# Optimization experiments

Measured on AMD Instinct MI355X. Metric: run time of the kernel, lower is better.

Reference implementation:

```python
import jax, jax.numpy as jnp
import numpy as np

# Production-scale dims (RecSys CTR): huge batch, modest feature dim -> memory-bound.
BATCH = 262144
DIM = 128
NUM_DOMAIN = 8
EPS = 1e-3  # Keras BatchNormalization default epsilon


def setup_inputs() -> dict:
    key = jax.random.key(0)
    k1, k2 = jax.random.split(key)
    inputs = jax.random.normal(k1, (BATCH, DIM), dtype=jnp.float32)
    domain_index = jax.random.randint(k2, (BATCH,), 0, NUM_DOMAIN, dtype=jnp.int32)
    # Learned params, matching Constant(0.5)/Zeros initializers in build().
    global_gamma = jnp.full((DIM,), 0.5, dtype=jnp.float32)
    global_beta = jnp.zeros((DIM,), dtype=jnp.float32)
    domain_gamma = jnp.full((NUM_DOMAIN, DIM), 0.5, dtype=jnp.float32)
    domain_beta = jnp.zeros((NUM_DOMAIN, DIM), dtype=jnp.float32)
    return {
        "inputs": inputs,
        "global_gamma": global_gamma,
        "global_beta": global_beta,
        "domain_gamma": domain_gamma,
        "domain_beta": domain_beta,
        "domain_index": domain_index,
    }


def reference(inputs, global_gamma, global_beta, domain_gamma, domain_beta, domain_index):
    """Partitioned Normalization (training-mode BN stats per domain).

    Equivalent to the per-domain loop of boolean_mask -> BatchNorm(center=False,
    scale=False) -> affine -> scatter, but expressed as one segmented reduction
    plus gathers (every row belongs to exactly one domain, so the scatter is a
    full per-row update).
    """
    seg = domain_index  # [B] int, values in [0, NUM_DOMAIN)
    ones = jnp.ones((inputs.shape[0],), dtype=inputs.dtype)
    counts = jax.ops.segment_sum(ones, seg, num_segments=NUM_DOMAIN)        # [K]
    sums = jax.ops.segment_sum(inputs, seg, num_segments=NUM_DOMAIN)        # [K, D]
    sqsums = jax.ops.segment_sum(inputs * inputs, seg, num_segments=NUM_DOMAIN)  # [K, D]
    n = jnp.maximum(counts, 1.0)[:, None]  # guard empty domains (their stats are unused)
    mean = sums / n                                        # [K, D] per-domain mean
    var = jnp.maximum(sqsums / n - mean * mean, 0.0)       # biased variance, as Keras BN
    # Normalize each row with its own domain's statistics (gather [B, D]).
    x_norm = (inputs - mean[seg]) * jax.lax.rsqrt(var[seg] + EPS)
    gamma = global_gamma + domain_gamma[seg]               # [B, D]
    beta = global_beta + domain_beta[seg]                  # [B, D]
    return gamma * x_norm + beta
```

## Files before the change

### kernel.cpp

```cpp
#include <hip/hip_runtime.h>
#include <hip/hip_bf16.h>


#define DIM 128
#define NDOM 8
#define PENT (NDOM + 2 * NDOM * DIM)
#define EPSV 1e-3f
#define WREG 2048

__global__ __launch_bounds__(256) void pn_reduce(const float4* __restrict__ x4,
                                                 const int* __restrict__ seg,
                                                 float* __restrict__ partials,
                                                 int rowsPerBlock) {
  __shared__ float acc[8 * WREG];
  __shared__ float lcnt[NDOM];
  const int tid = threadIdx.x;
  const int w = tid >> 6;
  const int l = tid & 63;
  const int h = l >> 5;
  const int g = l & 31;
  float* reg = acc + (w * 2 + h) * WREG;

  for (int i = tid; i < 2 * WREG; i += 256)
    ((float4*)acc)[i] = make_float4(0.f, 0.f, 0.f, 0.f);
  if (tid < NDOM) lcnt[tid] = 0.f;
  __syncthreads();

  const int rowsPerWave = rowsPerBlock >> 2;
  const int row0 = blockIdx.x * rowsPerBlock + w * rowsPerWave;

#define RMW(S, V)                                    \
  {                                                  \
    float* bs = reg + (S) * 128 + g * 4;             \
    float* bq = bs + NDOM * DIM;                     \
    float4 os = *(float4*)bs;                        \
    float4 oq = *(float4*)bq;                        \
    os.x += (V).x;                                   \
    os.y += (V).y;                                   \
    os.z += (V).z;                                   \
    os.w += (V).w;                                   \
    oq.x = fmaf((V).x, (V).x, oq.x);                 \
    oq.y = fmaf((V).y, (V).y, oq.y);                 \
    oq.z = fmaf((V).z, (V).z, oq.z);                 \
    oq.w = fmaf((V).w, (V).w, oq.w);                 \
    *(float4*)bs = os;                               \
    *(float4*)bq = oq;                               \
  }
  for (int it = 0; it < rowsPerWave; it += 8) {
    const int r = row0 + it;
    const int4 sgA = *(const int4*)(seg + r);
    const int4 sgB = *(const int4*)(seg + r + 4);
    const float4 v0 = x4[(size_t)(r + 0 + h) * 32 + g];
    const float4 v1 = x4[(size_t)(r + 2 + h) * 32 + g];
    const float4 v2 = x4[(size_t)(r + 4 + h) * 32 + g];
    const float4 v3 = x4[(size_t)(r + 6 + h) * 32 + g];
    const int s0 = h ? sgA.y : sgA.x;
    const int s1 = h ? sgA.w : sgA.z;
    const int s2 = h ? sgB.y : sgB.x;
    const int s3 = h ? sgB.w : sgB.z;
    RMW(s0, v0)
    RMW(s1, v1)
    RMW(s2, v2)
    RMW(s3, v3)
  }
#undef RMW
  __syncthreads();

  for (int i = tid; i < rowsPerBlock; i += 256)
    atomicAdd(&lcnt[seg[blockIdx.x * rowsPerBlock + i]], 1.f);
  __syncthreads();

  float* outp = partials + (size_t)blockIdx.x * PENT;
  if (tid < NDOM) outp[tid] = lcnt[tid];
  for (int i = tid; i < 2 * NDOM * DIM; i += 256) {
    float v = 0.f;
#pragma unroll
    for (int rr = 0; rr < 8; ++rr) v += acc[rr * WREG + i];
    outp[NDOM + i] = v;
  }
}

__global__ __launch_bounds__(256) void pn_reduce2(const float* __restrict__ partials,
                                                  float* __restrict__ partials2,
                                                  int NB) {
  const int b = blockIdx.x;
  const int per = NB >> 6;
  const int b0 = b * per;
  const int tid = threadIdx.x;
  float acc[9];
#pragma unroll
  for (int i = 0; i < 9; ++i) acc[i] = 0.f;
  for (int j = b0; j < b0 + per; ++j) {
    const float* p = partials + (size_t)j * PENT;
#pragma unroll
    for (int i = 0; i < 9; ++i) {
      const int e = tid + i * 256;
      if (e < PENT) acc[i] += p[e];
    }
  }
  float* o = partials2 + (size_t)b * PENT;
#pragma unroll
  for (int i = 0; i < 9; ++i) {
    const int e = tid + i * 256;
    if (e < PENT) o[e] = acc[i];
  }
}

__global__ __launch_bounds__(256) void pn_finalize(const float* __restrict__ partials2,
                                                   const float* __restrict__ gg,
                                                   const float* __restrict__ gb,
                                                   const float* __restrict__ dg,
                                                   const float* __restrict__ db,
                                                   float* __restrict__ stats) {
  const int t = blockIdx.x * 256 + threadIdx.x;
  const int k = t >> 7;
  const int d = t & (DIM - 1);
  float c = 0.f, s = 0.f, q = 0.f;
  for (int j = 0; j < 64; ++j) {
    const float* p = partials2 + (size_t)j * PENT;
    c += p[k];
    s += p[NDOM + t];
    q += p[NDOM + NDOM * DIM + t];
  }
  const float n = fmaxf(c, 1.f);
  const float mean = s / n;
  const float var = fmaxf(q / n - mean * mean, 0.f);
  const float rstd = rsqrtf(var + EPSV);
  const float scale = (gg[d] + dg[t]) * rstd;
  const float shift = (gb[d] + db[t]) - scale * mean;
  stats[t] = scale;
  stats[NDOM * DIM + t] = shift;
}

__global__ __launch_bounds__(256) void pn_apply(const float* __restrict__ x,
                                                const int* __restrict__ seg,
                                                const float* __restrict__ stats,
                                                float* __restrict__ out) {
  const int g = blockIdx.x * 256 + threadIdx.x;
  const int row = g >> 5;
  const int c4 = g & 31;
  const int s = seg[row];
  const float4 xv = ((const float4*)x)[g];
  const float4 a = ((const float4*)(stats + s * DIM))[c4];
  const float4 b = ((const float4*)(stats + NDOM * DIM + s * DIM))[c4];
  float4 o;
  o.x = fmaf(xv.x, a.x, b.x);
  o.y = fmaf(xv.y, a.y, b.y);
  o.z = fmaf(xv.z, a.z, b.z);
  o.w = fmaf(xv.w, a.w, b.w);
  ((float4*)out)[g] = o;
}

extern "C" void kernel_launch(void* const* d_in, const int* in_sizes, int n_in,
                              void* d_out, int out_size, void* d_ws, size_t ws_size,
                              hipStream_t stream) {
  const float* x = (const float*)d_in[0];
  const float* gg = (const float*)d_in[1];
  const float* gb = (const float*)d_in[2];
  const float* dg = (const float*)d_in[3];
  const float* db = (const float*)d_in[4];
  const int* seg = (const int*)d_in[5];
  float* out = (float*)d_out;
  const int B = in_sizes[5];

  const int NB = 512;
  float* partials = (float*)d_ws;
  float* partials2 = partials + (size_t)NB * PENT;
  float* stats = partials2 + (size_t)64 * PENT;

  const int rpb = B / NB;

  pn_reduce<<<NB, 256, 0, stream>>>((const float4*)x, seg, partials, rpb);
  pn_reduce2<<<64, 256, 0, stream>>>(partials, partials2, NB);
  pn_finalize<<<4, 256, 0, stream>>>(partials2, gg, gb, dg, db, stats);

  const int nblk = (B * (DIM / 4)) / 256;
  pn_apply<<<nblk, 256, 0, stream>>>(x, seg, stats, out);
}
```

Baseline: 91.75 us.

## Use float2 per-lane rows in reduce, halve shared accumulators, double blocks

In the reduction kernel each wave now covers a full row with 64 lanes reading float2, instead of two half-waves each reading float4. This halves the per-wave shared accumulator regions from 8 to 4, cutting shared memory from 64KB to 32KB so more blocks fit per CU, and the grid doubles to 1024 blocks. The trade-off is narrower loads, more LDS read-modify-write instructions per element, and twice as many partials for the second-stage reduce.

```diff
diff --git a/kernel.cpp b/kernel.cpp
--- a/kernel.cpp
+++ b/kernel.cpp
@@ -8,20 +8,18 @@
 #define EPSV 1e-3f
 #define WREG 2048
 
-__global__ __launch_bounds__(256) void pn_reduce(const float4* __restrict__ x4,
+__global__ __launch_bounds__(256) void pn_reduce(const float2* __restrict__ x2,
                                                  const int* __restrict__ seg,
                                                  float* __restrict__ partials,
                                                  int rowsPerBlock) {
-  __shared__ float acc[8 * WREG];
+  __shared__ float acc[4 * WREG];
   __shared__ float lcnt[NDOM];
   const int tid = threadIdx.x;
   const int w = tid >> 6;
   const int l = tid & 63;
-  const int h = l >> 5;
-  const int g = l & 31;
-  float* reg = acc + (w * 2 + h) * WREG;
+  float* reg = acc + w * WREG;
 
-  for (int i = tid; i < 2 * WREG; i += 256)
+  for (int i = tid; i < WREG; i += 256)
     ((float4*)acc)[i] = make_float4(0.f, 0.f, 0.f, 0.f);
   if (tid < NDOM) lcnt[tid] = 0.f;
   __syncthreads();
@@ -31,37 +29,37 @@
 
 #define RMW(S, V)                                    \
   {                                                  \
-    float* bs = reg + (S) * 128 + g * 4;             \
+    float* bs = reg + (S) * 128 + l * 2;             \
     float* bq = bs + NDOM * DIM;                     \
-    float4 os = *(float4*)bs;                        \
-    float4 oq = *(float4*)bq;                        \
+    float2 os = *(float2*)bs;                        \
+    float2 oq = *(float2*)bq;                        \
     os.x += (V).x;                                   \
     os.y += (V).y;                                   \
-    os.z += (V).z;                                   \
-    os.w += (V).w;                                   \
     oq.x = fmaf((V).x, (V).x, oq.x);                 \
     oq.y = fmaf((V).y, (V).y, oq.y);                 \
-    oq.z = fmaf((V).z, (V).z, oq.z);                 \
-    oq.w = fmaf((V).w, (V).w, oq.w);                 \
-    *(float4*)bs = os;                               \
-    *(float4*)bq = oq;                               \
+    *(float2*)bs = os;                               \
+    *(float2*)bq = oq;                               \
   }
   for (int it = 0; it < rowsPerWave; it += 8) {
     const int r = row0 + it;
     const int4 sgA = *(const int4*)(seg + r);
     const int4 sgB = *(const int4*)(seg + r + 4);
-    const float4 v0 = x4[(size_t)(r + 0 + h) * 32 + g];
-    const float4 v1 = x4[(size_t)(r + 2 + h) * 32 + g];
-    const float4 v2 = x4[(size_t)(r + 4 + h) * 32 + g];
-    const float4 v3 = x4[(size_t)(r + 6 + h) * 32 + g];
-    const int s0 = h ? sgA.y : sgA.x;
-    const int s1 = h ? sgA.w : sgA.z;
-    const int s2 = h ? sgB.y : sgB.x;
-    const int s3 = h ? sgB.w : sgB.z;
-    RMW(s0, v0)
-    RMW(s1, v1)
-    RMW(s2, v2)
-    RMW(s3, v3)
+    const float2 v0 = x2[(size_t)(r + 0) * 64 + l];
+    const float2 v1 = x2[(size_t)(r + 1) * 64 + l];
+    const float2 v2 = x2[(size_t)(r + 2) * 64 + l];
+    const float2 v3 = x2[(size_t)(r + 3) * 64 + l];
+    const float2 v4 = x2[(size_t)(r + 4) * 64 + l];
+    const float2 v5 = x2[(size_t)(r + 5) * 64 + l];
+    const float2 v6 = x2[(size_t)(r + 6) * 64 + l];
+    const float2 v7 = x2[(size_t)(r + 7) * 64 + l];
+    RMW(sgA.x, v0)
+    RMW(sgA.y, v1)
+    RMW(sgA.z, v2)
+    RMW(sgA.w, v3)
+    RMW(sgB.x, v4)
+    RMW(sgB.y, v5)
+    RMW(sgB.z, v6)
+    RMW(sgB.w, v7)
   }
 #undef RMW
   __syncthreads();
@@ -75,7 +73,7 @@
   for (int i = tid; i < 2 * NDOM * DIM; i += 256) {
     float v = 0.f;
 #pragma unroll
-    for (int rr = 0; rr < 8; ++rr) v += acc[rr * WREG + i];
+    for (int rr = 0; rr < 4; ++rr) v += acc[rr * WREG + i];
     outp[NDOM + i] = v;
   }
 }
@@ -163,14 +161,14 @@
   float* out = (float*)d_out;
   const int B = in_sizes[5];
 
-  const int NB = 512;
+  const int NB = 1024;
   float* partials = (float*)d_ws;
   float* partials2 = partials + (size_t)NB * PENT;
   float* stats = partials2 + (size_t)64 * PENT;
 
   const int rpb = B / NB;
 
-  pn_reduce<<<NB, 256, 0, stream>>>((const float4*)x, seg, partials, rpb);
+  pn_reduce<<<NB, 256, 0, stream>>>((const float2*)x, seg, partials, rpb);
   pn_reduce2<<<64, 256, 0, stream>>>(partials, partials2, NB);
   pn_finalize<<<4, 256, 0, stream>>>(partials2, gg, gb, dg, db, stats);
 
```

Result: slower. 97.81 us (+6.6%).
